# Performance work log

Hardware: AMD Instinct MI355X
Metric: run time of the kernel (lower is better)

## Reference

```python
import jax, jax.numpy as jnp
import numpy as np

B, S, D, P = 16, 128, 768, 1024
N_CLASSES = 121  # dataset != 'restaurant'


def setup_inputs() -> dict:
    key = jax.random.key(0)
    ks = jax.random.split(key, 8)
    scale = lambda fan_in: 1.0 / np.sqrt(fan_in)
    return {
        "spans_embedding": jax.random.normal(ks[0], (B, S, D), dtype=jnp.float32),
        "W1": jax.random.normal(ks[1], (3 * D, 2 * D), dtype=jnp.float32) * scale(3 * D),
        "b1": jnp.zeros((2 * D,), dtype=jnp.float32),
        "W2": jax.random.normal(ks[2], (2 * D, D), dtype=jnp.float32) * scale(2 * D),
        "b2": jnp.zeros((D,), dtype=jnp.float32),
        "W3": jax.random.normal(ks[3], (D, N_CLASSES), dtype=jnp.float32) * scale(D),
        "b3": jnp.zeros((N_CLASSES,), dtype=jnp.float32),
        "span_masks": jnp.ones((B, S), dtype=jnp.int32),
        "batch_idx": jax.random.randint(ks[4], (P,), 0, B, dtype=jnp.int64),
        "aspect_idx": jax.random.randint(ks[5], (P,), 0, S - 2, dtype=jnp.int64),
        "opinion_idx": jax.random.randint(ks[6], (P,), 0, S - 2, dtype=jnp.int64),
    }


def reference(spans_embedding, W1, b1, W2, b2, W3, b3,
              span_masks, batch_idx, aspect_idx, opinion_idx):
    S_ = spans_embedding.shape[1]
    pos = jnp.arange(S_)
    last = jnp.sum(span_masks, axis=1) - 1          # [B] last valid span index
    li = last[batch_idx]                             # [P]
    emb = spans_embedding[batch_idx]                 # [P, S, D] gathered per pair

    def rng_max(lo, hi):                             # max over spans in [lo, hi)
        mask = (pos[None, :] >= lo[:, None]) & (pos[None, :] < hi[:, None])
        return jnp.max(jnp.where(mask[:, :, None], emb, -jnp.inf), axis=1)

    def rng_mean(lo, hi):                            # mean over spans in [lo, hi)
        m = ((pos[None, :] >= lo[:, None]) & (pos[None, :] < hi[:, None])).astype(emb.dtype)
        cnt = jnp.maximum(jnp.sum(m, axis=1), 1.0)
        return jnp.einsum('ps,psd->pd', m, emb) / cnt[:, None]

    ones = jnp.ones_like(aspect_idx)
    # boundary index b: aspect when aspect!=0, else opinion (matches all non-both-zero branches)
    b = jnp.where(aspect_idx != 0, aspect_idx, opinion_idx)
    emb0 = spans_embedding[batch_idx, 0]             # [P, D]
    embL = spans_embedding[batch_idx, li]            # [P, D]
    left_nz = jnp.where((b == 1)[:, None], emb0, rng_max(ones, b))
    right_nz = jnp.where((b == li)[:, None], embL, rng_max(b, li))

    both0 = (aspect_idx == 0) & (opinion_idx == 0)
    left = jnp.where(both0[:, None], rng_mean(ones, li), left_nz)
    right = jnp.where(both0[:, None], rng_max(ones, li), right_nz)

    aspect_rep = spans_embedding[batch_idx, aspect_idx]
    o_eff = jnp.where(opinion_idx == 0, li, opinion_idx)
    opinion_rep = spans_embedding[batch_idx, o_eff]

    x = jnp.concatenate([aspect_rep + opinion_rep, left, right], axis=1)  # [P, 3D]
    h = jax.nn.relu(x @ W1 + b1)
    h = jax.nn.relu(h @ W2 + b2)
    return h @ W3 + b3                               # [P, n_classes]
```

## Files before the change

kernel.cpp:

```cpp
#include <hip/hip_runtime.h>
#include <hip/hip_bf16.h>
#include <math.h>

#define S_LEN 128
#define D_DIM 768
#define P_PAIRS 1024
#define B_BATCH 16

typedef __attribute__((ext_vector_type(8))) short bf16x8;
typedef __attribute__((ext_vector_type(4))) float f32x4;

#define PB_UNITS (B_BATCH * (D_DIM / 64))
#define T1_UNITS ((2304 / 64) * (1536 / 64))
#define T2_UNITS ((1536 / 64) * (768 / 64))
#define T3_UNITS ((768 / 64) * (128 / 64))

union SmemU {
    struct {
        ushort semb[128][64];
        ushort spref[128][64];
        ushort ssuf[128][64];
        ushort smean[64];
        float  lred[3][4][64];
        int    li;
    } pb;
    float t64[64][65];
};

__device__ __forceinline__ ushort f2bf(float f) {
    __hip_bfloat16 h = __float2bfloat16(f);
    return *(ushort*)&h;
}

__device__ __forceinline__ float bf2f(ushort u) {
    unsigned int x = ((unsigned int)u) << 16;
    float f;
    __builtin_memcpy(&f, &x, 4);
    return f;
}

__device__ __forceinline__ void gload16(const void* g, void* l) {
    __builtin_amdgcn_global_load_lds(
        (const __attribute__((address_space(1))) void*)g,
        (__attribute__((address_space(3))) void*)l, 16, 0, 0);
}

__global__ __launch_bounds__(256) void fused_prep_kernel(
    const float* __restrict__ emb_all,
    const int* __restrict__ span_masks,
    const int* __restrict__ batch_idx,
    const int* __restrict__ aspect_idx,
    const int* __restrict__ opinion_idx,
    ushort* __restrict__ X,
    const float* __restrict__ W1, ushort* __restrict__ W1t,
    const float* __restrict__ W2, ushort* __restrict__ W2t,
    const float* __restrict__ W3, ushort* __restrict__ W3t)
{
    __shared__ SmemU sm;
    int bid = blockIdx.x;
    int tid = threadIdx.x;

    if (bid < PB_UNITS) {
        int b = bid / (D_DIM / 64);
        int chunk = bid % (D_DIM / 64);
        int lane = tid & 63;
        int g = tid >> 6;
        int r0 = g * 32;
        int col = chunk * 64 + lane;

        if (tid == 0) {
            int s = 0;
            for (int i = 0; i < S_LEN; ++i) s += span_masks[b * S_LEN + i];
            sm.pb.li = s - 1;
        }
        __syncthreads();
        int li = sm.pb.li;

        const float* embb = emb_all + (size_t)b * S_LEN * D_DIM;

        float v[32];
        #pragma unroll
        for (int r = 0; r < 32; ++r) {
            v[r] = embb[(size_t)(r0 + r) * D_DIM + col];
            sm.pb.semb[r0 + r][lane] = f2bf(v[r]);
        }

        float wmax = -INFINITY, umax = -INFINITY, s = 0.f;
        #pragma unroll
        for (int r = 0; r < 32; ++r) {
            int gr = r0 + r;
            wmax = fmaxf(wmax, (gr == 0) ? -INFINITY : v[r]);
            bool in = (gr >= 1) && (gr < li);
            umax = fmaxf(umax, in ? v[r] : -INFINITY);
            s += in ? v[r] : 0.f;
        }
        sm.pb.lred[0][g][lane] = wmax;
        sm.pb.lred[1][g][lane] = umax;
        sm.pb.lred[2][g][lane] = s;
        __syncthreads();

        float basep = -INFINITY;
        #pragma unroll
        for (int gg = 0; gg < 3; ++gg)
            if (gg < g) basep = fmaxf(basep, sm.pb.lred[0][gg][lane]);
        float bases = -INFINITY;
        #pragma unroll
        for (int gg = 1; gg < 4; ++gg)
            if (gg > g) bases = fmaxf(bases, sm.pb.lred[1][gg][lane]);

        if (g == 0) {
            float tot = sm.pb.lred[2][0][lane] + sm.pb.lred[2][1][lane]
                      + sm.pb.lred[2][2][lane] + sm.pb.lred[2][3][lane];
            int cnt = (li - 1) > 0 ? (li - 1) : 1;
            sm.pb.smean[lane] = f2bf(tot / (float)cnt);
        }

        float m = basep;
        #pragma unroll
        for (int r = 0; r < 32; ++r) {
            int gr = r0 + r;
            m = fmaxf(m, (gr == 0) ? -INFINITY : v[r]);
            sm.pb.spref[gr][lane] = f2bf(m);
        }
        float m2 = bases;
        #pragma unroll
        for (int r = 31; r >= 0; --r) {
            int gr = r0 + r;
            bool in = (gr >= 1) && (gr < li);
            m2 = fmaxf(m2, in ? v[r] : -INFINITY);
            if (gr >= 1) sm.pb.ssuf[gr][lane] = f2bf(m2);
        }
        __syncthreads();

        int pbase = g * 256;
        for (int c = 0; c < 256; c += 64) {
            int p = pbase + c + lane;
            int vb = batch_idx[p];
            int va = aspect_idx[p];
            int vo = opinion_idx[p];
            unsigned long long mask = __ballot(vb == b);
            while (mask) {
                int i = __ffsll((long long)mask) - 1;
                mask &= mask - 1;
                int pp = pbase + c + i;
                int a = __shfl(va, i);
                int o = __shfl(vo, i);
                bool both0 = (a == 0) && (o == 0);
                int bnd = (a != 0) ? a : o;
                int oe = (o == 0) ? li : o;
                float ar  = bf2f(sm.pb.semb[a][lane]);
                float orp = bf2f(sm.pb.semb[oe][lane]);
                ushort left, right;
                if (both0) {
                    left  = sm.pb.smean[lane];
                    right = sm.pb.spref[li - 1][lane];
                } else {
                    left  = (bnd == 1)  ? sm.pb.semb[0][lane]
                                        : sm.pb.spref[bnd - 1][lane];
                    right = (bnd == li) ? sm.pb.semb[li][lane]
                                        : sm.pb.ssuf[bnd][lane];
                }
                size_t base = (size_t)pp * (3 * D_DIM) + col;
                X[base]             = f2bf(ar + orp);
                X[base + D_DIM]     = left;
                X[base + 2 * D_DIM] = right;
            }
        }
    } else {
        int tb = bid - PB_UNITS;
        const float* in; ushort* out; int K, N, Npad, bx, by;
        if (tb < T1_UNITS) {
            in = W1; out = W1t; K = 2304; N = 1536; Npad = 1536;
            bx = tb % (2304 / 64); by = tb / (2304 / 64);
        } else if (tb < T1_UNITS + T2_UNITS) {
            tb -= T1_UNITS;
            in = W2; out = W2t; K = 1536; N = 768; Npad = 768;
            bx = tb % (1536 / 64); by = tb / (1536 / 64);
        } else {
            tb -= T1_UNITS + T2_UNITS;
            in = W3; out = W3t; K = 768; N = 121; Npad = 128;
            bx = tb % (768 / 64); by = tb / (768 / 64);
        }
        int k0 = bx * 64, n0 = by * 64;

        int kr = tid >> 2;
        int nq = (tid & 3) * 16;
        if (n0 + 64 <= N) {
            #pragma unroll
            for (int j = 0; j < 4; ++j) {
                float4 vv = *(const float4*)&in[(size_t)(k0 + kr) * N + n0 + nq + j * 4];
                *(float4*)&sm.t64[kr][nq + j * 4] = vv;
            }
        } else {
            #pragma unroll
            for (int j = 0; j < 16; ++j) {
                int n = n0 + nq + j;
                sm.t64[kr][nq + j] = (n < N) ? in[(size_t)(k0 + kr) * N + n] : 0.f;
            }
        }
        __syncthreads();

        int nr = tid >> 2;
        int kq = (tid & 3) * 16;
        if (n0 + nr < Npad) {
            ushort tmp[16];
            #pragma unroll
            for (int j = 0; j < 16; ++j) tmp[j] = f2bf(sm.t64[kq + j][nr]);
            ushort* dst = out + (size_t)(n0 + nr) * K + k0 + kq;
            *(bf16x8*)dst       = *(bf16x8*)&tmp[0];
            *(bf16x8*)(dst + 8) = *(bf16x8*)&tmp[8];
        }
    }
}

template<int WRITE_BF16, int RELU>
__global__ __launch_bounds__(256, 3) void gemm_mfma(
    const ushort* __restrict__ A,
    const ushort* __restrict__ Bt,
    const float* __restrict__ bias,
    void* __restrict__ Cout,
    int M, int N, int K)
{
    __shared__ ushort lds[3][128 * 64];
    int tid = threadIdx.x;
    int lane = tid & 63;
    int w = tid >> 6;
    int wr = w >> 1, wc = w & 1;

    int gx = gridDim.x;
    int id = blockIdx.y * gx + blockIdx.x;
    int n8 = (gx * gridDim.y) >> 3;
    int swz = (id & 7) * n8 + (id >> 3);
    int bx = swz % gx;
    int by = swz / gx;

    int rowBase = by * 64;
    int colBase = bx * 64;

    int srow  = lane >> 3;
    int scolb = (((lane & 7) ^ srow) << 4);
    const char* Abase = (const char*)(A  + (size_t)rowBase * K);
    const char* Bbase = (const char*)(Bt + (size_t)colBase * K);
    size_t rstride = (size_t)K * 2;

    f32x4 acc[2][2] = {};
    int nt = K >> 6;

    auto stage = [&](int buf, int t) {
        size_t kb0 = (size_t)t << 7;
        #pragma unroll
        for (int i = 0; i < 2; ++i) {
            int r = w * 16 + i * 8 + srow;
            gload16(Abase + (size_t)r * rstride + kb0 + scolb,
                    &lds[buf][(w * 16 + i * 8) * 64]);
        }
        #pragma unroll
        for (int i = 0; i < 2; ++i) {
            int r = w * 16 + i * 8 + srow;
            gload16(Bbase + (size_t)r * rstride + kb0 + scolb,
                    &lds[buf][(64 + w * 16 + i * 8) * 64]);
        }
    };

    stage(0, 0);
    stage(1, 1);

    int cur = 0;
    for (int t = 0; t < nt; ++t) {
        if (t + 1 < nt) asm volatile("s_waitcnt vmcnt(4)" ::: "memory");
        else            asm volatile("s_waitcnt vmcnt(0)" ::: "memory");
        __builtin_amdgcn_s_barrier();
        __builtin_amdgcn_sched_barrier(0);

        if (t + 2 < nt) stage((t + 2) % 3, t + 2);

        const char* lb = (const char*)&lds[cur][0];
        int kq = (lane >> 4) << 4;
        bf16x8 af[2][2], bfr[2][2];
        #pragma unroll
        for (int m = 0; m < 2; ++m) {
            int row = wr * 32 + m * 16 + (lane & 15);
            #pragma unroll
            for (int kk = 0; kk < 2; ++kk) {
                int addr = row * 128 + ((kq + kk * 64) ^ ((row & 7) << 4));
                af[m][kk] = *(const bf16x8*)(lb + addr);
            }
        }
        #pragma unroll
        for (int n = 0; n < 2; ++n) {
            int row = 64 + wc * 32 + n * 16 + (lane & 15);
            #pragma unroll
            for (int kk = 0; kk < 2; ++kk) {
                int addr = row * 128 + ((kq + kk * 64) ^ ((row & 7) << 4));
                bfr[n][kk] = *(const bf16x8*)(lb + addr);
            }
        }
        __builtin_amdgcn_s_setprio(1);
        #pragma unroll
        for (int m = 0; m < 2; ++m)
            #pragma unroll
            for (int n = 0; n < 2; ++n)
                #pragma unroll
                for (int kk = 0; kk < 2; ++kk)
                    acc[m][n] = __builtin_amdgcn_mfma_f32_16x16x32_bf16(
                        af[m][kk], bfr[n][kk], acc[m][n], 0, 0, 0);
        __builtin_amdgcn_s_setprio(0);
        cur = (cur + 1) % 3;
    }

    #pragma unroll
    for (int m = 0; m < 2; ++m) {
        #pragma unroll
        for (int n = 0; n < 2; ++n) {
            #pragma unroll
            for (int j = 0; j < 4; ++j) {
                int row = rowBase + wr * 32 + m * 16 + (lane >> 4) * 4 + j;
                int col = colBase + wc * 32 + n * 16 + (lane & 15);
                if (col < N && row < M) {
                    float v = acc[m][n][j] + bias[col];
                    if (RELU) v = fmaxf(v, 0.f);
                    if (WRITE_BF16)
                        ((ushort*)Cout)[(size_t)row * N + col] = f2bf(v);
                    else
                        ((float*)Cout)[(size_t)row * N + col] = v;
                }
            }
        }
    }
}

extern "C" void kernel_launch(void* const* d_in, const int* in_sizes, int n_in,
                              void* d_out, int out_size, void* d_ws, size_t ws_size,
                              hipStream_t stream) {
    const float* emb        = (const float*)d_in[0];
    const float* W1         = (const float*)d_in[1];
    const float* b1         = (const float*)d_in[2];
    const float* W2         = (const float*)d_in[3];
    const float* b2         = (const float*)d_in[4];
    const float* W3         = (const float*)d_in[5];
    const float* b3         = (const float*)d_in[6];
    const int* span_masks   = (const int*)d_in[7];
    const int* batch_idx    = (const int*)d_in[8];
    const int* aspect_idx   = (const int*)d_in[9];
    const int* opinion_idx  = (const int*)d_in[10];
    float* out = (float*)d_out;

    ushort* Xb  = (ushort*)d_ws;
    ushort* H2  = Xb;
    ushort* W1t = Xb  + (size_t)1024 * 2304;
    ushort* W2t = W1t + (size_t)1536 * 2304;
    ushort* W3t = W2t + (size_t)768 * 1536;
    ushort* H1  = W3t + (size_t)128 * 768;

    fused_prep_kernel<<<PB_UNITS + T1_UNITS + T2_UNITS + T3_UNITS, 256, 0, stream>>>(
        emb, span_masks, batch_idx, aspect_idx, opinion_idx, Xb,
        W1, W1t, W2, W2t, W3, W3t);

    gemm_mfma<1,1><<<dim3(1536/64, 1024/64), 256, 0, stream>>>(Xb, W1t, b1, H1, 1024, 1536, 2304);
    gemm_mfma<1,1><<<dim3( 768/64, 1024/64), 256, 0, stream>>>(H1, W2t, b2, H2, 1024, 768, 1536);
    gemm_mfma<0,0><<<dim3( 128/64, 1024/64), 256, 0, stream>>>(H2, W3t, b3, out, 1024, 121, 768);
}
```

Measured before the change: 55.33 us.

## Use 64x96 output tiles for first MLP GEMM to fit grid to one wave

After: 56.06 us. No clear change (+1.3%).

```diff
diff --git a/kernel.cpp b/kernel.cpp
--- a/kernel.cpp
+++ b/kernel.cpp
@@ -214,6 +214,117 @@
 }
 
 template<int WRITE_BF16, int RELU>
+__global__ __launch_bounds__(256) void gemm_mfma96(
+    const ushort* __restrict__ A,
+    const ushort* __restrict__ Bt,
+    const float* __restrict__ bias,
+    void* __restrict__ Cout,
+    int M, int N, int K)
+{
+    __shared__ ushort lds[3][160 * 64];
+    int tid = threadIdx.x;
+    int lane = tid & 63;
+    int w = tid >> 6;
+    int wr = w >> 1, wc = w & 1;
+    int rl = lane & 15;
+
+    int id = blockIdx.y * 16 + blockIdx.x;
+    int swz = (id & 7) * 32 + (id >> 3);
+    int bx = swz % 16;
+    int by = swz / 16;
+
+    int rowBase = by * 64;
+    int colBase = bx * 96;
+
+    int srow  = lane >> 3;
+    int scolb = (((lane & 7) ^ srow) << 4);
+    const char* Abase = (const char*)(A  + (size_t)rowBase * K);
+    const char* Bbase = (const char*)(Bt + (size_t)colBase * K);
+    size_t rstride = (size_t)K * 2;
+    const char* Badj = Bbase - (size_t)64 * rstride;
+
+    f32x4 acc[2][3] = {};
+    int nt = K >> 6;
+
+    auto stage = [&](int buf, int t) {
+        size_t kb0 = (size_t)t << 7;
+        #pragma unroll
+        for (int i = 0; i < 5; ++i) {
+            int g = w * 5 + i;
+            const char* eb = (g < 8) ? Abase : Badj;
+            gload16(eb + (size_t)(g * 8 + srow) * rstride + kb0 + scolb,
+                    &lds[buf][g * 512]);
+        }
+    };
+
+    stage(0, 0);
+    stage(1, 1);
+
+    int cur = 0;
+    for (int t = 0; t < nt; ++t) {
+        if (t + 1 < nt) asm volatile("s_waitcnt vmcnt(5)" ::: "memory");
+        else            asm volatile("s_waitcnt vmcnt(0)" ::: "memory");
+        __builtin_amdgcn_s_barrier();
+        __builtin_amdgcn_sched_barrier(0);
+
+        if (t + 2 < nt) stage((t + 2) % 3, t + 2);
+
+        const char* lb = (const char*)&lds[cur][0];
+        int kq = (lane >> 4) << 4;
+        bf16x8 af[2][2], bfr[3][2];
+        #pragma unroll
+        for (int m = 0; m < 2; ++m) {
+            int row = wr * 32 + m * 16 + rl;
+            #pragma unroll
+            for (int kk = 0; kk < 2; ++kk) {
+                int addr = row * 128 + ((kq + kk * 64) ^ ((row & 7) << 4));
+                af[m][kk] = *(const bf16x8*)(lb + addr);
+            }
+        }
+        #pragma unroll
+        for (int n = 0; n < 3; ++n) {
+            int row = 64 + wc * 48 + n * 16 + rl;
+            #pragma unroll
+            for (int kk = 0; kk < 2; ++kk) {
+                int addr = row * 128 + ((kq + kk * 64) ^ ((row & 7) << 4));
+                bfr[n][kk] = *(const bf16x8*)(lb + addr);
+            }
+        }
+        __builtin_amdgcn_s_setprio(1);
+        #pragma unroll
+        for (int m = 0; m < 2; ++m)
+            #pragma unroll
+            for (int n = 0; n < 3; ++n)
+                #pragma unroll
+                for (int kk = 0; kk < 2; ++kk)
+                    acc[m][n] = __builtin_amdgcn_mfma_f32_16x16x32_bf16(
+                        af[m][kk], bfr[n][kk], acc[m][n], 0, 0, 0);
+        __builtin_amdgcn_s_setprio(0);
+        cur = (cur + 1) % 3;
+    }
+
+    #pragma unroll
+    for (int m = 0; m < 2; ++m) {
+        #pragma unroll
+        for (int n = 0; n < 3; ++n) {
+            #pragma unroll
+            for (int j = 0; j < 4; ++j) {
+                int row = rowBase + wr * 32 + m * 16 + (lane >> 4) * 4 + j;
+                int col = colBase + wc * 48 + n * 16 + rl;
+                if (col < N && row < M) {
+                    float v = acc[m][n][j] + bias[col];
+                    if (RELU) v = fmaxf(v, 0.f);
+                    if (WRITE_BF16)
+                        ((ushort*)Cout)[(size_t)row * N + col] = f2bf(v);
+                    else
+                        ((float*)Cout)[(size_t)row * N + col] = v;
+                }
+            }
+        }
+    }
+}
+
+template<int WRITE_BF16, int RELU>
 __global__ __launch_bounds__(256, 3) void gemm_mfma(
     const ushort* __restrict__ A,
     const ushort* __restrict__ Bt,
@@ -356,7 +467,7 @@
         emb, span_masks, batch_idx, aspect_idx, opinion_idx, Xb,
         W1, W1t, W2, W2t, W3, W3t);
 
-    gemm_mfma<1,1><<<dim3(1536/64, 1024/64), 256, 0, stream>>>(Xb, W1t, b1, H1, 1024, 1536, 2304);
-    gemm_mfma<1,1><<<dim3( 768/64, 1024/64), 256, 0, stream>>>(H1, W2t, b2, H2, 1024, 768, 1536);
-    gemm_mfma<0,0><<<dim3( 128/64, 1024/64), 256, 0, stream>>>(H2, W3t, b3, out, 1024, 121, 768);
-}
+    gemm_mfma96<1,1><<<dim3(1536/96, 1024/64), 256, 0, stream>>>(Xb, W1t, b1, H1, 1024, 1536, 2304);
+    gemm_mfma  <1,1><<<dim3( 768/64, 1024/64), 256, 0, stream>>>(H1, W2t, b2, H2, 1024, 768, 1536);
+    gemm_mfma  <0,0><<<dim3( 128/64, 1024/64), 256, 0, stream>>>(H2, W3t, b3, out, 1024, 121, 768);
+}
```
